# Performance work log

Measured on AMD Instinct MI355X. Metric: run time of the kernel, lower is better.

The kernel has to match this reference:

```python
import jax, jax.numpy as jnp
import numpy as np

Nc, Nq = 100000, 20000
Fc, Fq = 300, 768
HID, H, L = 128, 4, 2
D = HID // H
OUT = 8
E = 400000
NT, ET = 2, 3


def setup_inputs() -> dict:
    key = jax.random.key(0)
    ks = jax.random.split(key, 24)
    def n(i, shape, s=1.0):
        return jax.random.normal(ks[i], shape, dtype=jnp.float32) * s
    return {
        'x_context': n(0, (Nc, Fc)),
        'x_question': n(1, (Nq, Fq)),
        'src_q2c': jax.random.randint(ks[2], (E,), 0, Nq),
        'dst_q2c': jax.random.randint(ks[3], (E,), 0, Nc),
        'src_c2c': jax.random.randint(ks[4], (E,), 0, Nc),
        'dst_c2c': jax.random.randint(ks[5], (E,), 0, Nc),
        'src_c2q': jax.random.randint(ks[6], (E,), 0, Nc),
        'dst_c2q': jax.random.randint(ks[7], (E,), 0, Nq),
        'in_W_context': n(8, (Fc, HID), 0.05),
        'in_b_context': jnp.zeros((HID,), jnp.float32),
        'in_W_question': n(9, (Fq, HID), 0.05),
        'in_b_question': jnp.zeros((HID,), jnp.float32),
        'k_W': n(10, (L, NT, HID, HID), 0.05),
        'k_b': jnp.zeros((L, NT, HID), jnp.float32),
        'q_W': n(11, (L, NT, HID, HID), 0.05),
        'q_b': jnp.zeros((L, NT, HID), jnp.float32),
        'v_W': n(12, (L, NT, HID, HID), 0.05),
        'v_b': jnp.zeros((L, NT, HID), jnp.float32),
        'a_W': n(13, (L, NT, HID, HID), 0.05),
        'a_b': jnp.zeros((L, NT, HID), jnp.float32),
        'skip': jnp.ones((L, NT), jnp.float32),
        'a_rel': n(14, (L, ET, H, D, D), 0.1),
        'm_rel': n(15, (L, ET, H, D, D), 0.1),
        'p_rel': jnp.ones((L, ET, H), jnp.float32),
        'out_W': n(16, (HID, OUT), 0.05),
        'out_b': jnp.zeros((OUT,), jnp.float32),
    }


def segment_softmax(logits, seg, num):
    # logits: [E, H], seg: [E] destination node ids
    m = jax.ops.segment_max(logits, seg, num_segments=num)
    m = jnp.where(jnp.isfinite(m), m, 0.0)
    e = jnp.exp(logits - m[seg])
    s = jax.ops.segment_sum(e, seg, num_segments=num)
    return e / (s[seg] + 1e-16)


def reference(x_context, x_question, src_q2c, dst_q2c, src_c2c, dst_c2c,
              src_c2q, dst_c2q, in_W_context, in_b_context, in_W_question,
              in_b_question, k_W, k_b, q_W, q_b, v_W, v_b, a_W, a_b, skip,
              a_rel, m_rel, p_rel, out_W, out_b):
    # node type 0 = 'context', 1 = 'question'
    x = [jax.nn.relu(x_context @ in_W_context + in_b_context),
         jax.nn.relu(x_question @ in_W_question + in_b_question)]
    Ns = [x[0].shape[0], x[1].shape[0]]
    # (src_nt, dst_nt, src_idx, dst_idx) per edge type
    edge_types = [(1, 0, src_q2c, dst_q2c),
                  (0, 0, src_c2c, dst_c2c),
                  (0, 1, src_c2q, dst_c2q)]
    scale = 1.0 / jnp.sqrt(jnp.float32(D))
    for l in range(L):
        k = [(x[nt] @ k_W[l, nt] + k_b[l, nt]).reshape(-1, H, D) for nt in range(NT)]
        q = [(x[nt] @ q_W[l, nt] + q_b[l, nt]).reshape(-1, H, D) for nt in range(NT)]
        v = [(x[nt] @ v_W[l, nt] + v_b[l, nt]).reshape(-1, H, D) for nt in range(NT)]
        agg = [jnp.zeros((Ns[nt], H, D), x[0].dtype) for nt in range(NT)]
        for et, (snt, dnt, src, dst) in enumerate(edge_types):
            k_rel = jnp.einsum('ehd,hdf->ehf', k[snt][src], a_rel[l, et])
            v_rel = jnp.einsum('ehd,hdf->ehf', v[snt][src], m_rel[l, et])
            logits = jnp.einsum('ehd,ehd->eh', q[dnt][dst], k_rel) * p_rel[l, et] * scale
            alpha = segment_softmax(logits, dst, Ns[dnt])  # [E, H]
            agg[dnt] = agg[dnt].at[dst].add(v_rel * alpha[:, :, None])
        for nt in range(NT):
            o = jax.nn.gelu(agg[nt].reshape(Ns[nt], HID), approximate=False)
            o = o @ a_W[l, nt] + a_b[l, nt]
            g = jax.nn.sigmoid(skip[l, nt])
            x[nt] = g * o + (1.0 - g) * x[nt]
    return x[0] @ out_W + out_b
```

## Files before the change

### kernel.cpp

```cpp
#include <hip/hip_runtime.h>

constexpr int NC = 100000;
constexpr int NQ = 20000;
constexpr int FC = 300;
constexpr int FQ = 768;
constexpr int NEDGE = 400000;
constexpr int NTOT = NC + NC + NQ;
constexpr int NTOT2 = NC + NQ;
constexpr int NB0 = (NC + 127) / 128;
constexpr int NB1 = (NQ + 127) / 128;
constexpr int NBALL = NB0 + NB1;
constexpr float SCALE = 0.17677669529663687f;
constexpr float LOG2E = 1.4426950408889634f;

typedef __attribute__((ext_vector_type(8))) short bf16x8;
typedef __attribute__((ext_vector_type(4))) float f32x4;
typedef unsigned short u16;

__device__ __forceinline__ float gelu_f(float x) {
  return 0.5f * x * (1.0f + erff(x * 0.7071067811865476f));
}
__device__ __forceinline__ u16 bf16_rne(float x) {
  unsigned u = __float_as_uint(x);
  unsigned r = u + 0x7fffu + ((u >> 16) & 1u);
  return (u16)(r >> 16);
}
__device__ __forceinline__ float bf16_to_f(u16 h) {
  return __uint_as_float(((unsigned)h) << 16);
}
__device__ __forceinline__ void split2(float x, u16& hi, u16& lo) {
  hi = bf16_rne(x);
  lo = bf16_rne(x - bf16_to_f(hi));
}
__device__ __forceinline__ void splitT(float x, u16& hi, u16& lo) {
  hi = (u16)(__float_as_uint(x) >> 16);
  lo = bf16_rne(x - bf16_to_f(hi));
}

__global__ void k_count3(const int* __restrict__ d0, const int* __restrict__ d1,
                         const int* __restrict__ d2, int* __restrict__ counts) {
  int i = blockIdx.x * 256 + threadIdx.x;
  if (i >= 3 * NEDGE) return;
  int et = i / NEDGE, e = i - et * NEDGE;
  int d = (et == 0) ? d0[e] : (et == 1) ? d1[e] : d2[e];
  int base = (et == 0) ? 0 : (et == 1) ? NC : 2 * NC;
  atomicAdd(&counts[base + d], 1);
}

__global__ void k_scan_block(const int* __restrict__ in, int* __restrict__ out,
                             int* __restrict__ bsum, int n) {
  __shared__ int s[256];
  int tid = threadIdx.x;
  int i = blockIdx.x * 256 + tid;
  int v = (i < n) ? in[i] : 0;
  s[tid] = v;
  __syncthreads();
  for (int off = 1; off < 256; off <<= 1) {
    int t = (tid >= off) ? s[tid - off] : 0;
    __syncthreads();
    s[tid] += t;
    __syncthreads();
  }
  if (i < n) out[i] = s[tid] - v;
  if (tid == 255) bsum[blockIdx.x] = s[255];
}

__global__ void k_scan_sums(int* __restrict__ bsum, int nb) {
  __shared__ int s[1024];
  int tid = threadIdx.x;
  int v = (tid < nb) ? bsum[tid] : 0;
  s[tid] = v;
  __syncthreads();
  for (int off = 1; off < 1024; off <<= 1) {
    int t = (tid >= off) ? s[tid - off] : 0;
    __syncthreads();
    s[tid] += t;
    __syncthreads();
  }
  if (tid < nb) bsum[tid] = s[tid] - v;
}

__global__ void k_scan_add(int* __restrict__ ptr, const int* __restrict__ bsum,
                           int* __restrict__ cursor, int n, int total) {
  int i = blockIdx.x * 256 + threadIdx.x;
  if (i < n) {
    int v = ptr[i] + bsum[blockIdx.x];
    ptr[i] = v;
    cursor[i] = v;
  }
  if (i == 0) ptr[n] = total;
}

__global__ void k_scatter3(const int* __restrict__ s0, const int* __restrict__ s1,
                           const int* __restrict__ s2, const int* __restrict__ d0,
                           const int* __restrict__ d1, const int* __restrict__ d2,
                           int* __restrict__ cursor, int* __restrict__ srcs_out) {
  int i = blockIdx.x * 256 + threadIdx.x;
  if (i >= 3 * NEDGE) return;
  int et = i / NEDGE, e = i - et * NEDGE;
  int d = (et == 0) ? d0[e] : (et == 1) ? d1[e] : d2[e];
  int sv = (et == 0) ? s0[e] : (et == 1) ? s1[e] : s2[e];
  int base = (et == 0) ? 0 : (et == 1) ? NC : 2 * NC;
  int p = atomicAdd(&cursor[base + d], 1);
  srcs_out[p] = sv;
}

__global__ void prep_all(const float* __restrict__ kW, const float* __restrict__ kB,
                         const float* __restrict__ qW, const float* __restrict__ qB,
                         const float* __restrict__ vW, const float* __restrict__ vB,
                         const float* __restrict__ aW, const float* __restrict__ aB,
                         const float* __restrict__ arel, const float* __restrict__ mrel,
                         const float* __restrict__ prel,
                         u16* __restrict__ Bth, u16* __restrict__ Btl,
                         float* __restrict__ biasOut) {
  int i = blockIdx.x;
  int col = threadIdx.x;
  int y = blockIdx.y;
  int l = y / 10, yy = y % 10;
  size_t lw = (size_t)l * 2 * 16384, lb = (size_t)l * 2 * 128;
  size_t le = (size_t)l * 3 * 4096, lp = (size_t)l * 3 * 4;
  const float *W = nullptr, *bb = nullptr, *rel = nullptr, *pr = nullptr;
  float mscale = 1.0f;
  bool fold = false;
  switch (yy) {
    case 0: W = qW + lw; bb = qB + lb; break;
    case 1: fold = true; W = kW + lw; bb = kB + lb; rel = arel + le + 4096; pr = prel + lp + 4; mscale = SCALE; break;
    case 2: fold = true; W = vW + lw; bb = vB + lb; rel = mrel + le + 4096; break;
    case 3: fold = true; W = kW + lw; bb = kB + lb; rel = arel + le + 8192; pr = prel + lp + 8; mscale = SCALE; break;
    case 4: fold = true; W = vW + lw; bb = vB + lb; rel = mrel + le + 8192; break;
    case 5: W = qW + lw + 16384; bb = qB + lb + 128; break;
    case 6: fold = true; W = kW + lw + 16384; bb = kB + lb + 128; rel = arel + le; pr = prel + lp; mscale = SCALE; break;
    case 7: fold = true; W = vW + lw + 16384; bb = vB + lb + 128; rel = mrel + le; break;
    case 8: W = aW + lw; bb = aB + lb; break;
    default: W = aW + lw + 16384; bb = aB + lb + 128; break;
  }
  int colOff = y * 128;
  if (!fold) {
    float v = W[i * 128 + col];
    u16 hi, lo;
    split2(v, hi, lo);
    Bth[(size_t)(colOff + col) * 128 + i] = hi;
    Btl[(size_t)(colOff + col) * 128 + i] = lo;
    if (i == 0) biasOut[colOff + col] = bb[col];
    return;
  }
  int h = col >> 5, f = col & 31;
  float m = (pr ? pr[h] : 1.0f) * mscale;
  float s = 0.0f;
  #pragma unroll
  for (int d = 0; d < 32; ++d)
    s += W[i * 128 + h * 32 + d] * rel[(h * 32 + d) * 32 + f];
  s *= m;
  u16 hi, lo;
  split2(s, hi, lo);
  Bth[(size_t)(colOff + col) * 128 + i] = hi;
  Btl[(size_t)(colOff + col) * 128 + i] = lo;
  if (i == 0) {
    float sb = 0.0f;
    #pragma unroll
    for (int d = 0; d < 32; ++d)
      sb += bb[h * 32 + d] * rel[(h * 32 + d) * 32 + f];
    biasOut[colOff + col] = sb * m;
  }
}

__global__ void split_in(const float* __restrict__ Wc, const float* __restrict__ bc,
                         const float* __restrict__ Wq, const float* __restrict__ bq,
                         u16* __restrict__ Bth, u16* __restrict__ Btl,
                         float* __restrict__ biasOut) {
  int n = blockIdx.x, y = blockIdx.y;
  const float* W = y ? Wq : Wc;
  const float* b = y ? bq : bc;
  int K = y ? FQ : FC, Kp = y ? 768 : 320;
  size_t boff = y ? (size_t)128 * 320 : 0;
  for (int k = threadIdx.x; k < Kp; k += 256) {
    float v = (k < K) ? W[(size_t)k * 128 + n] : 0.0f;
    u16 hi, lo;
    split2(v, hi, lo);
    Bth[boff + (size_t)n * Kp + k] = hi;
    Btl[boff + (size_t)n * Kp + k] = lo;
  }
  if (threadIdx.x == 0) biasOut[(y ? 128 : 0) + n] = b[n];
}

__global__ __launch_bounds__(256) void big_gemm(
    const float* __restrict__ Ac, const float* __restrict__ Aq,
    const u16* __restrict__ Bth, const u16* __restrict__ Btl,
    const float* __restrict__ biasBuf,
    u16* __restrict__ xh_all, u16* __restrict__ xl_all) {
  __shared__ u16 smem[20480];
  constexpr int AHo = 0, ALo = 5120, BHo = 10240, BLo = 15360;
  const int tid = threadIdx.x, lane = tid & 63, wv = tid >> 6;
  const int l15 = lane & 15, g4 = lane >> 4, koff = g4 * 8;
  const int sr = tid >> 1, sc16 = (tid & 1) * 16;

  const int bid = blockIdx.x;
  const int nt = (bid < NB0) ? 0 : 1;
  const int m0 = nt ? (bid - NB0) * 128 : bid * 128;
  const int M = nt ? NQ : NC;
  const int rowbase = nt ? NC : 0;
  const float* A32;
  int K, Kp, biasOff;
  size_t boff;
  if (nt == 0) { A32 = Ac; K = FC; Kp = 320; boff = 0; biasOff = 0; }
  else { A32 = Aq; K = FQ; Kp = 768; boff = (size_t)128 * 320; biasOff = 128; }
  size_t arow = (size_t)(m0 + sr) * K;
  const bool rowokA = (m0 + sr) < M;

  f32x4 acc[2][8];
  #pragma unroll
  for (int mi = 0; mi < 2; ++mi)
    #pragma unroll
    for (int ni = 0; ni < 8; ++ni) acc[mi][ni] = (f32x4){0.f, 0.f, 0.f, 0.f};

  for (int k0 = 0; k0 < K; k0 += 32) {
    float va[16];
    if (rowokA && (k0 + 32 <= K)) {
      const float* ap = A32 + arow + k0 + sc16;
      #pragma unroll
      for (int j = 0; j < 4; ++j) {
        float4 f = *(const float4*)(ap + 4 * j);
        va[4 * j + 0] = f.x; va[4 * j + 1] = f.y; va[4 * j + 2] = f.z; va[4 * j + 3] = f.w;
      }
    } else {
      #pragma unroll
      for (int j = 0; j < 16; ++j) {
        int kc = k0 + sc16 + j;
        va[j] = (rowokA && kc < K) ? A32[arow + kc] : 0.0f;
      }
    }
    {
      alignas(16) u16 hv[16], lv[16];
      #pragma unroll
      for (int j = 0; j < 16; ++j) splitT(va[j], hv[j], lv[j]);
      *(uint4*)&smem[AHo + sr * 40 + sc16] = *(const uint4*)&hv[0];
      *(uint4*)&smem[AHo + sr * 40 + sc16 + 8] = *(const uint4*)&hv[8];
      *(uint4*)&smem[ALo + sr * 40 + sc16] = *(const uint4*)&lv[0];
      *(uint4*)&smem[ALo + sr * 40 + sc16 + 8] = *(const uint4*)&lv[8];
    }
    {
      const u16* bp = Bth + boff + (size_t)sr * Kp + k0 + sc16;
      *(uint4*)&smem[BHo + sr * 40 + sc16] = *(const uint4*)bp;
      *(uint4*)&smem[BHo + sr * 40 + sc16 + 8] = *(const uint4*)(bp + 8);
      const u16* lp = Btl + boff + (size_t)sr * Kp + k0 + sc16;
      *(uint4*)&smem[BLo + sr * 40 + sc16] = *(const uint4*)lp;
      *(uint4*)&smem[BLo + sr * 40 + sc16 + 8] = *(const uint4*)(lp + 8);
    }
    __syncthreads();

    bf16x8 a_h[2], a_l[2];
    #pragma unroll
    for (int mi = 0; mi < 2; ++mi) {
      int row = wv * 32 + mi * 16 + l15;
      a_h[mi] = *(const bf16x8*)&smem[AHo + row * 40 + koff];
      a_l[mi] = *(const bf16x8*)&smem[ALo + row * 40 + koff];
    }
    #pragma unroll
    for (int ni = 0; ni < 8; ++ni) {
      int col = ni * 16 + l15;
      bf16x8 b_h = *(const bf16x8*)&smem[BHo + col * 40 + koff];
      bf16x8 b_l = *(const bf16x8*)&smem[BLo + col * 40 + koff];
      #pragma unroll
      for (int mi = 0; mi < 2; ++mi) {
        acc[mi][ni] = __builtin_amdgcn_mfma_f32_16x16x32_bf16(a_h[mi], b_h, acc[mi][ni], 0, 0, 0);
        acc[mi][ni] = __builtin_amdgcn_mfma_f32_16x16x32_bf16(a_l[mi], b_h, acc[mi][ni], 0, 0, 0);
        acc[mi][ni] = __builtin_amdgcn_mfma_f32_16x16x32_bf16(a_h[mi], b_l, acc[mi][ni], 0, 0, 0);
      }
    }
    __syncthreads();
  }

  #pragma unroll
  for (int mi = 0; mi < 2; ++mi)
    #pragma unroll
    for (int ni = 0; ni < 8; ++ni) {
      float bi = biasBuf[biasOff + ni * 16 + l15];
      #pragma unroll
      for (int rr = 0; rr < 4; ++rr)
        acc[mi][ni][rr] = fmaxf(acc[mi][ni][rr] + bi, 0.0f);
    }

  const int wrow = tid >> 2, wseg = tid & 3;
  #pragma unroll
  for (int ph = 0; ph < 2; ++ph) {
    #pragma unroll
    for (int h = 0; h < 2; ++h) {
      if (ph || h) __syncthreads();
      if ((wv >> 1) == h) {
        #pragma unroll
        for (int mi = 0; mi < 2; ++mi) {
          int rl = (wv & 1) * 32 + mi * 16 + g4 * 4;
          #pragma unroll
          for (int ni = 0; ni < 8; ++ni) {
            #pragma unroll
            for (int rr = 0; rr < 4; ++rr) {
              u16 hh, ll;
              split2(acc[mi][ni][rr], hh, ll);
              smem[(rl + rr) * 136 + ni * 16 + l15] = ph ? ll : hh;
            }
          }
        }
      }
      __syncthreads();
      int grow = m0 + h * 64 + wrow;
      if (grow < M) {
        u16* dstp = ph ? xl_all : xh_all;
        uint4* dst = (uint4*)&dstp[(size_t)(rowbase + grow) * 128 + wseg * 32];
        const uint4* src = (const uint4*)&smem[wrow * 136 + wseg * 32];
        #pragma unroll
        for (int j = 0; j < 4; ++j) dst[j] = src[j];
      }
    }
  }
}

__global__ __launch_bounds__(256) void aproj_gemm(
    const u16* __restrict__ Ag,
    const u16* __restrict__ Bth, const u16* __restrict__ Btl,
    const float* __restrict__ biasBuf,
    u16* __restrict__ xh_all, u16* __restrict__ xl_all,
    const float* __restrict__ skip, int l) {
  __shared__ u16 smem[15360];
  constexpr int AH = 0, BHo = 5120, BLo = 10240;
  const int tid = threadIdx.x, lane = tid & 63, wv = tid >> 6;
  const int l15 = lane & 15, g4 = lane >> 4, koff = g4 * 8;
  const int sr = tid >> 1, sc = (tid & 1) * 16;

  const int bid = blockIdx.x;
  const int nt = (bid < NB0) ? 0 : 1;
  const int m0 = nt ? (bid - NB0) * 128 : bid * 128;
  const int M = nt ? NQ : NC;
  const int rowbase = nt ? NC : 0;
  const size_t boff = (size_t)(8 + nt) * 16384;
  const int biasOff = (8 + nt) * 128;
  const bool rowok = (m0 + sr) < M;

  f32x4 acc[2][8];
  #pragma unroll
  for (int mi = 0; mi < 2; ++mi)
    #pragma unroll
    for (int ni = 0; ni < 8; ++ni) acc[mi][ni] = (f32x4){0.f, 0.f, 0.f, 0.f};

  for (int k0 = 0; k0 < 128; k0 += 32) {
    uint4 h0 = {0, 0, 0, 0}, h1 = {0, 0, 0, 0};
    if (rowok) {
      const u16* ap = Ag + (size_t)(rowbase + m0 + sr) * 128 + k0 + sc;
      h0 = *(const uint4*)ap;
      h1 = *(const uint4*)(ap + 8);
    }
    *(uint4*)&smem[AH + sr * 40 + sc] = h0;
    *(uint4*)&smem[AH + sr * 40 + sc + 8] = h1;
    {
      const u16* bp = Bth + boff + (size_t)sr * 128 + k0 + sc;
      *(uint4*)&smem[BHo + sr * 40 + sc] = *(const uint4*)bp;
      *(uint4*)&smem[BHo + sr * 40 + sc + 8] = *(const uint4*)(bp + 8);
      const u16* lp = Btl + boff + (size_t)sr * 128 + k0 + sc;
      *(uint4*)&smem[BLo + sr * 40 + sc] = *(const uint4*)lp;
      *(uint4*)&smem[BLo + sr * 40 + sc + 8] = *(const uint4*)(lp + 8);
    }
    __syncthreads();

    bf16x8 a_h[2];
    #pragma unroll
    for (int mi = 0; mi < 2; ++mi) {
      int row = wv * 32 + mi * 16 + l15;
      a_h[mi] = *(const bf16x8*)&smem[AH + row * 40 + koff];
    }
    #pragma unroll
    for (int ni = 0; ni < 8; ++ni) {
      int col = ni * 16 + l15;
      bf16x8 b_h = *(const bf16x8*)&smem[BHo + col * 40 + koff];
      bf16x8 b_l = *(const bf16x8*)&smem[BLo + col * 40 + koff];
      #pragma unroll
      for (int mi = 0; mi < 2; ++mi) {
        acc[mi][ni] = __builtin_amdgcn_mfma_f32_16x16x32_bf16(a_h[mi], b_h, acc[mi][ni], 0, 0, 0);
        acc[mi][ni] = __builtin_amdgcn_mfma_f32_16x16x32_bf16(a_h[mi], b_l, acc[mi][ni], 0, 0, 0);
      }
    }
    __syncthreads();
  }

  float g = 1.0f / (1.0f + __expf(-skip[l * 2 + nt]));

  #pragma unroll
  for (int mi = 0; mi < 2; ++mi) {
    #pragma unroll
    for (int ni = 0; ni < 8; ++ni) {
      int colL = ni * 16 + l15;
      float bi = biasBuf[biasOff + colL];
      #pragma unroll
      for (int rr = 0; rr < 4; ++rr) {
        int row = m0 + wv * 32 + mi * 16 + g4 * 4 + rr;
        float o = acc[mi][ni][rr] + bi;
        if (row < M) {
          size_t idx = (size_t)(rowbase + row) * 128 + colL;
          float xo = bf16_to_f(xh_all[idx]) + bf16_to_f(xl_all[idx]);
          o = g * o + (1.0f - g) * xo;
        }
        acc[mi][ni][rr] = o;
      }
    }
  }

  const int wrow = tid >> 2, wseg = tid & 3;
  #pragma unroll
  for (int ph = 0; ph < 2; ++ph) {
    #pragma unroll
    for (int h = 0; h < 2; ++h) {
      if (ph || h) __syncthreads();
      if ((wv >> 1) == h) {
        #pragma unroll
        for (int mi = 0; mi < 2; ++mi) {
          int rl = (wv & 1) * 32 + mi * 16 + g4 * 4;
          #pragma unroll
          for (int ni = 0; ni < 8; ++ni) {
            #pragma unroll
            for (int rr = 0; rr < 4; ++rr) {
              u16 hh, ll;
              split2(acc[mi][ni][rr], hh, ll);
              smem[(rl + rr) * 136 + ni * 16 + l15] = ph ? ll : hh;
            }
          }
        }
      }
      __syncthreads();
      int grow = m0 + h * 64 + wrow;
      if (grow < M) {
        u16* dstp = ph ? xl_all : xh_all;
        uint4* dst = (uint4*)&dstp[(size_t)(rowbase + grow) * 128 + wseg * 32];
        const uint4* src = (const uint4*)&smem[wrow * 136 + wseg * 32];
        #pragma unroll
        for (int j = 0; j < 4; ++j) dst[j] = src[j];
      }
    }
  }
}

__global__ __launch_bounds__(256) void proj_all(
    const u16* __restrict__ xh_all,
    const u16* __restrict__ Bth, const float* __restrict__ biasBuf,
    u16* __restrict__ q_all, u16* __restrict__ kvA,
    u16* __restrict__ kvB1, u16* __restrict__ kvB2, int last) {
  int bid = blockIdx.x, y = blockIdx.y;
  int nt = (bid < NB0) ? 0 : 1;
  if (nt == 1 && y >= 3) return;
  if (last) {
    if (nt == 0 && y >= 3) return;
    if (nt == 1 && y == 0) return;
  }
  __shared__ u16 smem[10240];
  constexpr int AH = 0, BH = 5120;
  int m0 = nt ? (bid - NB0) * 128 : bid * 128;
  int M = nt ? NQ : NC;
  int abase = nt ? NC : 0;
  int bslab = nt ? 5 + y : y;
  u16* cp; int ld, cb, crowbase;
  if (nt == 0) {
    switch (y) {
      case 0: cp = q_all; ld = 128; cb = 0; crowbase = 0; break;
      case 1: cp = kvB1; ld = 256; cb = 0; crowbase = 0; break;
      case 2: cp = kvB1; ld = 256; cb = 128; crowbase = 0; break;
      case 3: cp = kvB2; ld = 256; cb = 0; crowbase = 0; break;
      default: cp = kvB2; ld = 256; cb = 128; crowbase = 0; break;
    }
  } else {
    switch (y) {
      case 0: cp = q_all; ld = 128; cb = 0; crowbase = NC; break;
      case 1: cp = kvA; ld = 256; cb = 0; crowbase = 0; break;
      default: cp = kvA; ld = 256; cb = 128; crowbase = 0; break;
    }
  }
  const int tid = threadIdx.x, lane = tid & 63, wv = tid >> 6;
  const int l15 = lane & 15, g4 = lane >> 4, koff = g4 * 8;
  const int sr = tid >> 1, sc = (tid & 1) * 16;
  const bool rowok = (m0 + sr) < M;

  f32x4 acc[2][8];
  #pragma unroll
  for (int mi = 0; mi < 2; ++mi)
    #pragma unroll
    for (int ni = 0; ni < 8; ++ni) acc[mi][ni] = (f32x4){0.f, 0.f, 0.f, 0.f};

  for (int k0 = 0; k0 < 128; k0 += 32) {
    uint4 h0 = {0, 0, 0, 0}, h1 = {0, 0, 0, 0};
    if (rowok) {
      const u16* ap = xh_all + (size_t)(abase + m0 + sr) * 128 + k0 + sc;
      h0 = *(const uint4*)ap;
      h1 = *(const uint4*)(ap + 8);
    }
    *(uint4*)&smem[AH + sr * 40 + sc] = h0;
    *(uint4*)&smem[AH + sr * 40 + sc + 8] = h1;
    {
      const u16* bp = Bth + (size_t)(bslab * 128 + sr) * 128 + k0 + sc;
      *(uint4*)&smem[BH + sr * 40 + sc] = *(const uint4*)bp;
      *(uint4*)&smem[BH + sr * 40 + sc + 8] = *(const uint4*)(bp + 8);
    }
    __syncthreads();

    bf16x8 a_h[2];
    #pragma unroll
    for (int mi = 0; mi < 2; ++mi) {
      int row = wv * 32 + mi * 16 + l15;
      a_h[mi] = *(const bf16x8*)&smem[AH + row * 40 + koff];
    }
    #pragma unroll
    for (int ni = 0; ni < 8; ++ni) {
      int col = ni * 16 + l15;
      bf16x8 b_h = *(const bf16x8*)&smem[BH + col * 40 + koff];
      #pragma unroll
      for (int mi = 0; mi < 2; ++mi)
        acc[mi][ni] = __builtin_amdgcn_mfma_f32_16x16x32_bf16(a_h[mi], b_h, acc[mi][ni], 0, 0, 0);
    }
    __syncthreads();
  }

  const int wrow = tid >> 2, wseg = tid & 3;
  #pragma unroll
  for (int h = 0; h < 2; ++h) {
    if (h) __syncthreads();
    if ((wv >> 1) == h) {
      #pragma unroll
      for (int mi = 0; mi < 2; ++mi) {
        int rl = (wv & 1) * 32 + mi * 16 + g4 * 4;
        #pragma unroll
        for (int ni = 0; ni < 8; ++ni) {
          float bi = biasBuf[bslab * 128 + ni * 16 + l15];
          #pragma unroll
          for (int rr = 0; rr < 4; ++rr)
            smem[(rl + rr) * 136 + ni * 16 + l15] = bf16_rne(acc[mi][ni][rr] + bi);
        }
      }
    }
    __syncthreads();
    int grow = m0 + h * 64 + wrow;
    if (grow < M) {
      uint4* dst = (uint4*)&cp[(size_t)(crowbase + grow) * ld + cb + wseg * 32];
      const uint4* src = (const uint4*)&smem[wrow * 136 + wseg * 32];
      #pragma unroll
      for (int j = 0; j < 4; ++j) dst[j] = src[j];
    }
  }
}

__device__ __forceinline__ void attn_seg(
    const u16* __restrict__ kv, int start, int end,
    const int* __restrict__ srcs, const float q8[8], int lane, float accO[8]) {
  if (start >= end) return;
  float sum = 0.0f;
  float acc[8];
  #pragma unroll
  for (int i = 0; i < 8; ++i) acc[i] = 0.0f;
  const int half = lane >> 5;
  const int sub = lane & 31;
  const int bsrc = lane & 44;
  for (int e = start; e < end; e += 4) {
    int e0 = e + half;
    int e1 = e + 2 + half;
    bool v0 = e0 < end, v1 = e1 < end;
    int c0 = v0 ? e0 : end - 1;
    int c1 = v1 ? e1 : end - 1;
    int s0 = srcs[c0];
    int s1 = srcs[c1];
    uint4 u0 = *(const uint4*)&kv[(size_t)s0 * 256 + sub * 8];
    uint4 u1 = *(const uint4*)&kv[(size_t)s1 * 256 + sub * 8];
    float r0[8], r1[8];
    r0[0] = bf16_to_f((u16)(u0.x & 0xffffu)); r0[1] = bf16_to_f((u16)(u0.x >> 16));
    r0[2] = bf16_to_f((u16)(u0.y & 0xffffu)); r0[3] = bf16_to_f((u16)(u0.y >> 16));
    r0[4] = bf16_to_f((u16)(u0.z & 0xffffu)); r0[5] = bf16_to_f((u16)(u0.z >> 16));
    r0[6] = bf16_to_f((u16)(u0.w & 0xffffu)); r0[7] = bf16_to_f((u16)(u0.w >> 16));
    r1[0] = bf16_to_f((u16)(u1.x & 0xffffu)); r1[1] = bf16_to_f((u16)(u1.x >> 16));
    r1[2] = bf16_to_f((u16)(u1.y & 0xffffu)); r1[3] = bf16_to_f((u16)(u1.y >> 16));
    r1[4] = bf16_to_f((u16)(u1.z & 0xffffu)); r1[5] = bf16_to_f((u16)(u1.z >> 16));
    r1[6] = bf16_to_f((u16)(u1.w & 0xffffu)); r1[7] = bf16_to_f((u16)(u1.w >> 16));
    float p0 = q8[0] * r0[0];
    float p1 = q8[0] * r1[0];
    #pragma unroll
    for (int i = 1; i < 8; ++i) {
      p0 = fmaf(q8[i], r0[i], p0);
      p1 = fmaf(q8[i], r1[i], p1);
    }
    p0 += __shfl_xor(p0, 1);
    p1 += __shfl_xor(p1, 1);
    p0 += __shfl_xor(p0, 2);
    p1 += __shfl_xor(p1, 2);
    p0 = fminf(p0, 100.0f);
    p1 = fminf(p1, 100.0f);
    float w0 = v0 ? exp2f(p0) : 0.0f;
    float w1 = v1 ? exp2f(p1) : 0.0f;
    float wB0 = __shfl(w0, bsrc);
    float wB1 = __shfl(w1, bsrc);
    sum += wB0 + wB1;
    #pragma unroll
    for (int i = 0; i < 8; ++i) {
      acc[i] = fmaf(wB0, r0[i], acc[i]);
      acc[i] = fmaf(wB1, r1[i], acc[i]);
    }
  }
  sum += __shfl_xor(sum, 32);
  #pragma unroll
  for (int i = 0; i < 8; ++i) acc[i] += __shfl_xor(acc[i], 32);
  float inv = 1.0f / (sum + 1e-16f);
  #pragma unroll
  for (int i = 0; i < 8; ++i) accO[i] = fmaf(acc[i], inv, accO[i]);
}

__global__ __launch_bounds__(256) void attn_all(
    const u16* __restrict__ q_all, const u16* __restrict__ kvA,
    const u16* __restrict__ kvB1, const u16* __restrict__ kvB2,
    const int* __restrict__ ptr_all, const int* __restrict__ srcs_all,
    u16* __restrict__ agg_g, int ncap) {
  int wave = threadIdx.x >> 6, lane = threadIdx.x & 63;
  int node = blockIdx.x * 4 + wave;
  if (node >= ncap) return;
  int sub = lane & 31;
  float q8[8];
  #pragma unroll
  for (int i = 0; i < 8; ++i) q8[i] = 0.0f;
  if (sub < 16) {
    uint4 u = *(const uint4*)&q_all[(size_t)node * 128 + sub * 8];
    q8[0] = bf16_to_f((u16)(u.x & 0xffffu)) * LOG2E; q8[1] = bf16_to_f((u16)(u.x >> 16)) * LOG2E;
    q8[2] = bf16_to_f((u16)(u.y & 0xffffu)) * LOG2E; q8[3] = bf16_to_f((u16)(u.y >> 16)) * LOG2E;
    q8[4] = bf16_to_f((u16)(u.z & 0xffffu)) * LOG2E; q8[5] = bf16_to_f((u16)(u.z >> 16)) * LOG2E;
    q8[6] = bf16_to_f((u16)(u.w & 0xffffu)) * LOG2E; q8[7] = bf16_to_f((u16)(u.w >> 16)) * LOG2E;
  }
  float accO[8];
  #pragma unroll
  for (int i = 0; i < 8; ++i) accO[i] = 0.0f;
  if (node < NC) {
    attn_seg(kvA, ptr_all[node], ptr_all[node + 1], srcs_all, q8, lane, accO);
    attn_seg(kvB1, ptr_all[NC + node], ptr_all[NC + node + 1], srcs_all, q8, lane, accO);
  } else {
    int idx = 2 * NC + (node - NC);
    attn_seg(kvB2, ptr_all[idx], ptr_all[idx + 1], srcs_all, q8, lane, accO);
  }
  if (lane >= 16 && lane < 32) {
    int j = lane - 16;
    alignas(16) u16 hv[8];
    #pragma unroll
    for (int i = 0; i < 8; ++i) hv[i] = bf16_rne(gelu_f(accO[i]));
    *(uint4*)&agg_g[(size_t)node * 128 + j * 8] = *(const uint4*)hv;
  }
}

__global__ __launch_bounds__(256) void gemm_out(const u16* __restrict__ Xh,
                                                const u16* __restrict__ Xl,
                                                const float* __restrict__ W,
                                                const float* __restrict__ b,
                                                float* __restrict__ out, int M) {
  __shared__ float Ws[1024];
  __shared__ float As[32][129];
  int tid = threadIdx.x;
  int m0 = blockIdx.x * 32;
  *(float4*)&Ws[tid * 4] = *(const float4*)&W[tid * 4];
  {
    int r = tid >> 3;
    int c0 = (tid & 7) * 16;
    if (m0 + r < M) {
      const u16* hp = Xh + (size_t)(m0 + r) * 128 + c0;
      const u16* lp = Xl + (size_t)(m0 + r) * 128 + c0;
      #pragma unroll
      for (int j = 0; j < 16; ++j) As[r][c0 + j] = bf16_to_f(hp[j]) + bf16_to_f(lp[j]);
    } else {
      #pragma unroll
      for (int j = 0; j < 16; ++j) As[r][c0 + j] = 0.0f;
    }
  }
  __syncthreads();
  int r = tid >> 3, c = tid & 7;
  float sum = b[c];
  #pragma unroll 16
  for (int k = 0; k < 128; ++k) sum = fmaf(As[r][k], Ws[k * 8 + c], sum);
  if (m0 + r < M) out[(size_t)(m0 + r) * 8 + c] = sum;
}

static inline size_t align256(size_t x) { return (x + 255) & ~(size_t)255; }

extern "C" void kernel_launch(void* const* d_in, const int* in_sizes, int n_in,
                              void* d_out, int out_size, void* d_ws, size_t ws_size,
                              hipStream_t stream) {
  const float* x_context = (const float*)d_in[0];
  const float* x_question = (const float*)d_in[1];
  const int* src_q2c = (const int*)d_in[2];
  const int* dst_q2c = (const int*)d_in[3];
  const int* src_c2c = (const int*)d_in[4];
  const int* dst_c2c = (const int*)d_in[5];
  const int* src_c2q = (const int*)d_in[6];
  const int* dst_c2q = (const int*)d_in[7];
  const float* inWc = (const float*)d_in[8];
  const float* inbc = (const float*)d_in[9];
  const float* inWq = (const float*)d_in[10];
  const float* inbq = (const float*)d_in[11];
  const float* kW = (const float*)d_in[12];
  const float* kB = (const float*)d_in[13];
  const float* qW = (const float*)d_in[14];
  const float* qB = (const float*)d_in[15];
  const float* vW = (const float*)d_in[16];
  const float* vB = (const float*)d_in[17];
  const float* aW = (const float*)d_in[18];
  const float* aB = (const float*)d_in[19];
  const float* skip = (const float*)d_in[20];
  const float* arel = (const float*)d_in[21];
  const float* mrel = (const float*)d_in[22];
  const float* prel = (const float*)d_in[23];
  const float* outW = (const float*)d_in[24];
  const float* outb = (const float*)d_in[25];

  char* base = (char*)d_ws;
  size_t off = 0;
  auto carve = [&](size_t bytes) -> void* {
    void* p = base + off;
    off = align256(off + bytes);
    return p;
  };
  u16* xh_all = (u16*)carve((size_t)NTOT2 * 128 * 2);
  u16* xl_all = (u16*)carve((size_t)NTOT2 * 128 * 2);
  u16* q_all = (u16*)carve((size_t)NTOT2 * 128 * 2);
  u16* kvA = (u16*)carve((size_t)NQ * 256 * 2);
  u16* kvB1 = (u16*)carve((size_t)NC * 256 * 2);
  u16* kvB2 = (u16*)carve((size_t)NC * 256 * 2);
  u16* agg_g = (u16*)carve((size_t)NTOT2 * 128 * 2);
  u16* Bth = (u16*)carve((size_t)2560 * 128 * 2);
  u16* Btl = (u16*)carve((size_t)2560 * 128 * 2);
  u16* BthI = (u16*)carve((size_t)(320 + 768) * 128 * 2);
  u16* BtlI = (u16*)carve((size_t)(320 + 768) * 128 * 2);
  float* biasBuf = (float*)carve(2560 * 4);
  float* biasIn = (float*)carve(256 * 4);
  int* ptr_all = (int*)carve((size_t)(NTOT + 1) * 4);
  int* srcs_all = (int*)carve((size_t)3 * NEDGE * 4);
  int* counts = (int*)carve((size_t)NTOT * 4);
  int* cursor = (int*)carve((size_t)NTOT * 4);
  int* blksums = (int*)carve(2048 * 4);

  {
    int nb = (NTOT + 255) / 256;
    hipMemsetAsync(counts, 0, (size_t)NTOT * 4, stream);
    k_count3<<<(3 * NEDGE + 255) / 256, 256, 0, stream>>>(dst_q2c, dst_c2c, dst_c2q, counts);
    k_scan_block<<<nb, 256, 0, stream>>>(counts, ptr_all, blksums, NTOT);
    k_scan_sums<<<1, 1024, 0, stream>>>(blksums, nb);
    k_scan_add<<<nb, 256, 0, stream>>>(ptr_all, blksums, cursor, NTOT, 3 * NEDGE);
    k_scatter3<<<(3 * NEDGE + 255) / 256, 256, 0, stream>>>(
        src_q2c, src_c2c, src_c2q, dst_q2c, dst_c2c, dst_c2q, cursor, srcs_all);
  }

  split_in<<<dim3(128, 2), 256, 0, stream>>>(inWc, inbc, inWq, inbq, BthI, BtlI, biasIn);
  prep_all<<<dim3(128, 20), 128, 0, stream>>>(kW, kB, qW, qB, vW, vB, aW, aB,
                                              arel, mrel, prel, Bth, Btl, biasBuf);

  big_gemm<<<NBALL, 256, 0, stream>>>(x_context, x_question, BthI, BtlI, biasIn,
                                      xh_all, xl_all);

  for (int l = 0; l < 2; ++l) {
    const int last = (l == 1);
    const u16* BthL = Bth + (size_t)l * 10 * 128 * 128;
    const u16* BtlL = Btl + (size_t)l * 10 * 128 * 128;
    const float* biasL = biasBuf + (size_t)l * 1280;
    proj_all<<<dim3(NBALL, 5), 256, 0, stream>>>(xh_all, BthL, biasL,
                                                 q_all, kvA, kvB1, kvB2, last);
    int ncap = last ? NC : NTOT2;
    attn_all<<<(ncap + 3) / 4, 256, 0, stream>>>(q_all, kvA, kvB1, kvB2,
                                                 ptr_all, srcs_all, agg_g, ncap);
    aproj_gemm<<<last ? NB0 : NBALL, 256, 0, stream>>>(agg_g, BthL, BtlL, biasL,
                                                       xh_all, xl_all, skip, l);
  }

  gemm_out<<<(NC + 31) / 32, 256, 0, stream>>>(xh_all, xl_all, outW, outb, (float*)d_out, NC);
}
```

Baseline: 728.8 us.

## Load activation tile once and loop over weight slabs in projection kernel

The projection kernel now stages each block's 128x128 activation tile into shared memory once and iterates over all needed weight slabs (q, k, v per edge type) inside the block, instead of launching a separate block per slab that reloads the activation tile. This cuts repeated global reads of activations and the number of blocks, at the cost of larger shared memory use and fewer blocks per launch. The counts memset is also folded into the weight-prep kernel, which is moved ahead of the CSR build to save one launch.

```diff
diff --git a/kernel.cpp b/kernel.cpp
--- a/kernel.cpp
+++ b/kernel.cpp
@@ -112,10 +112,14 @@
                          const float* __restrict__ arel, const float* __restrict__ mrel,
                          const float* __restrict__ prel,
                          u16* __restrict__ Bth, u16* __restrict__ Btl,
-                         float* __restrict__ biasOut) {
+                         float* __restrict__ biasOut, int* __restrict__ counts) {
   int i = blockIdx.x;
   int col = threadIdx.x;
   int y = blockIdx.y;
+  {
+    int gid = (y * 128 + i) * 128 + col;
+    if (gid < NTOT) counts[gid] = 0;
+  }
   int l = y / 10, yy = y % 10;
   size_t lw = (size_t)l * 2 * 16384, lb = (size_t)l * 2 * 128;
   size_t le = (size_t)l * 3 * 4096, lp = (size_t)l * 3 * 4;
@@ -436,108 +440,115 @@
   }
 }
 
-__global__ __launch_bounds__(256) void proj_all(
+__global__ __launch_bounds__(256) void projN(
     const u16* __restrict__ xh_all,
     const u16* __restrict__ Bth, const float* __restrict__ biasBuf,
     u16* __restrict__ q_all, u16* __restrict__ kvA,
     u16* __restrict__ kvB1, u16* __restrict__ kvB2, int last) {
-  int bid = blockIdx.x, y = blockIdx.y;
-  int nt = (bid < NB0) ? 0 : 1;
-  if (nt == 1 && y >= 3) return;
-  if (last) {
-    if (nt == 0 && y >= 3) return;
-    if (nt == 1 && y == 0) return;
-  }
-  __shared__ u16 smem[10240];
-  constexpr int AH = 0, BH = 5120;
-  int m0 = nt ? (bid - NB0) * 128 : bid * 128;
-  int M = nt ? NQ : NC;
-  int abase = nt ? NC : 0;
-  int bslab = nt ? 5 + y : y;
-  u16* cp; int ld, cb, crowbase;
-  if (nt == 0) {
-    switch (y) {
-      case 0: cp = q_all; ld = 128; cb = 0; crowbase = 0; break;
-      case 1: cp = kvB1; ld = 256; cb = 0; crowbase = 0; break;
-      case 2: cp = kvB1; ld = 256; cb = 128; crowbase = 0; break;
-      case 3: cp = kvB2; ld = 256; cb = 0; crowbase = 0; break;
-      default: cp = kvB2; ld = 256; cb = 128; crowbase = 0; break;
-    }
-  } else {
-    switch (y) {
-      case 0: cp = q_all; ld = 128; cb = 0; crowbase = NC; break;
-      case 1: cp = kvA; ld = 256; cb = 0; crowbase = 0; break;
-      default: cp = kvA; ld = 256; cb = 128; crowbase = 0; break;
-    }
-  }
+  __shared__ u16 smem[22528];
+  constexpr int AH = 0, BH = 17408;
   const int tid = threadIdx.x, lane = tid & 63, wv = tid >> 6;
   const int l15 = lane & 15, g4 = lane >> 4, koff = g4 * 8;
-  const int sr = tid >> 1, sc = (tid & 1) * 16;
-  const bool rowok = (m0 + sr) < M;
-
-  f32x4 acc[2][8];
-  #pragma unroll
-  for (int mi = 0; mi < 2; ++mi)
-    #pragma unroll
-    for (int ni = 0; ni < 8; ++ni) acc[mi][ni] = (f32x4){0.f, 0.f, 0.f, 0.f};
-
-  for (int k0 = 0; k0 < 128; k0 += 32) {
-    uint4 h0 = {0, 0, 0, 0}, h1 = {0, 0, 0, 0};
-    if (rowok) {
-      const u16* ap = xh_all + (size_t)(abase + m0 + sr) * 128 + k0 + sc;
-      h0 = *(const uint4*)ap;
-      h1 = *(const uint4*)(ap + 8);
-    }
-    *(uint4*)&smem[AH + sr * 40 + sc] = h0;
-    *(uint4*)&smem[AH + sr * 40 + sc + 8] = h1;
-    {
-      const u16* bp = Bth + (size_t)(bslab * 128 + sr) * 128 + k0 + sc;
-      *(uint4*)&smem[BH + sr * 40 + sc] = *(const uint4*)bp;
-      *(uint4*)&smem[BH + sr * 40 + sc + 8] = *(const uint4*)(bp + 8);
-    }
-    __syncthreads();
-
-    bf16x8 a_h[2];
-    #pragma unroll
-    for (int mi = 0; mi < 2; ++mi) {
-      int row = wv * 32 + mi * 16 + l15;
-      a_h[mi] = *(const bf16x8*)&smem[AH + row * 40 + koff];
-    }
-    #pragma unroll
-    for (int ni = 0; ni < 8; ++ni) {
-      int col = ni * 16 + l15;
-      bf16x8 b_h = *(const bf16x8*)&smem[BH + col * 40 + koff];
-      #pragma unroll
-      for (int mi = 0; mi < 2; ++mi)
-        acc[mi][ni] = __builtin_amdgcn_mfma_f32_16x16x32_bf16(a_h[mi], b_h, acc[mi][ni], 0, 0, 0);
-    }
-    __syncthreads();
-  }
-
-  const int wrow = tid >> 2, wseg = tid & 3;
-  #pragma unroll
-  for (int h = 0; h < 2; ++h) {
-    if (h) __syncthreads();
-    if ((wv >> 1) == h) {
+  const int bid = blockIdx.x;
+  const int nt = (bid < NB0) ? 0 : 1;
+  const int m0 = nt ? (bid - NB0) * 128 : bid * 128;
+  const int M = nt ? NQ : NC;
+  const int abase = nt ? NC : 0;
+  const int nslab = nt ? (last ? 2 : 3) : (last ? 3 : 5);
+
+  {
+    const int sr = tid >> 1, sc = (tid & 1) * 64;
+    if ((m0 + sr) < M) {
+      const u16* ap = xh_all + (size_t)(abase + m0 + sr) * 128 + sc;
+      #pragma unroll
+      for (int j = 0; j < 8; ++j)
+        *(uint4*)&smem[AH + sr * 136 + sc + j * 8] = *(const uint4*)(ap + j * 8);
+    } else {
+      uint4 z = {0, 0, 0, 0};
+      #pragma unroll
+      for (int j = 0; j < 8; ++j)
+        *(uint4*)&smem[AH + sr * 136 + sc + j * 8] = z;
+    }
+  }
+
+  const int srB = tid >> 1, scB = (tid & 1) * 16;
+  for (int s = 0; s < nslab; ++s) {
+    int y = (nt == 1 && last) ? (s + 1) : s;
+    int bslab = nt ? 5 + y : y;
+    u16* cp; int ld, cb, crowbase;
+    if (nt == 0) {
+      switch (y) {
+        case 0: cp = q_all; ld = 128; cb = 0; crowbase = 0; break;
+        case 1: cp = kvB1; ld = 256; cb = 0; crowbase = 0; break;
+        case 2: cp = kvB1; ld = 256; cb = 128; crowbase = 0; break;
+        case 3: cp = kvB2; ld = 256; cb = 0; crowbase = 0; break;
+        default: cp = kvB2; ld = 256; cb = 128; crowbase = 0; break;
+      }
+    } else {
+      switch (y) {
+        case 0: cp = q_all; ld = 128; cb = 0; crowbase = NC; break;
+        case 1: cp = kvA; ld = 256; cb = 0; crowbase = 0; break;
+        default: cp = kvA; ld = 256; cb = 128; crowbase = 0; break;
+      }
+    }
+
+    f32x4 acc[2][8];
+    #pragma unroll
+    for (int mi = 0; mi < 2; ++mi)
+      #pragma unroll
+      for (int ni = 0; ni < 8; ++ni) acc[mi][ni] = (f32x4){0.f, 0.f, 0.f, 0.f};
+
+    #pragma unroll
+    for (int ks = 0; ks < 4; ++ks) {
+      const u16* bp = Bth + (size_t)(bslab * 128 + srB) * 128 + ks * 32 + scB;
+      uint4 b0 = *(const uint4*)bp;
+      uint4 b1 = *(const uint4*)(bp + 8);
+      __syncthreads();
+      *(uint4*)&smem[BH + srB * 40 + scB] = b0;
+      *(uint4*)&smem[BH + srB * 40 + scB + 8] = b1;
+      __syncthreads();
+
+      bf16x8 a_h[2];
       #pragma unroll
       for (int mi = 0; mi < 2; ++mi) {
-        int rl = (wv & 1) * 32 + mi * 16 + g4 * 4;
+        int row = wv * 32 + mi * 16 + l15;
+        a_h[mi] = *(const bf16x8*)&smem[AH + row * 136 + ks * 32 + koff];
+      }
+      #pragma unroll
+      for (int ni = 0; ni < 8; ++ni) {
+        int col = ni * 16 + l15;
+        bf16x8 b_h = *(const bf16x8*)&smem[BH + col * 40 + koff];
         #pragma unroll
-        for (int ni = 0; ni < 8; ++ni) {
-          float bi = biasBuf[bslab * 128 + ni * 16 + l15];
+        for (int mi = 0; mi < 2; ++mi)
+          acc[mi][ni] = __builtin_amdgcn_mfma_f32_16x16x32_bf16(a_h[mi], b_h, acc[mi][ni], 0, 0, 0);
+      }
+    }
+
+    #pragma unroll
+    for (int h = 0; h < 4; ++h) {
+      __syncthreads();
+      if (wv == h) {
+        #pragma unroll
+        for (int mi = 0; mi < 2; ++mi) {
+          int rl = mi * 16 + g4 * 4;
           #pragma unroll
-          for (int rr = 0; rr < 4; ++rr)
-            smem[(rl + rr) * 136 + ni * 16 + l15] = bf16_rne(acc[mi][ni][rr] + bi);
+          for (int ni = 0; ni < 8; ++ni) {
+            float bi = biasBuf[bslab * 128 + ni * 16 + l15];
+            #pragma unroll
+            for (int rr = 0; rr < 4; ++rr)
+              smem[BH + (rl + rr) * 136 + ni * 16 + l15] = bf16_rne(acc[mi][ni][rr] + bi);
+          }
         }
       }
-    }
-    __syncthreads();
-    int grow = m0 + h * 64 + wrow;
-    if (grow < M) {
-      uint4* dst = (uint4*)&cp[(size_t)(crowbase + grow) * ld + cb + wseg * 32];
-      const uint4* src = (const uint4*)&smem[wrow * 136 + wseg * 32];
-      #pragma unroll
-      for (int j = 0; j < 4; ++j) dst[j] = src[j];
+      __syncthreads();
+      int r = tid >> 3, cseg = (tid & 7) * 16;
+      int grow = m0 + h * 32 + r;
+      if (grow < M) {
+        uint4* dst = (uint4*)&cp[(size_t)(crowbase + grow) * ld + cb + cseg];
+        const uint4* src = (const uint4*)&smem[BH + r * 136 + cseg];
+        dst[0] = src[0];
+        dst[1] = src[1];
+      }
     }
   }
 }
@@ -731,9 +742,12 @@
   int* cursor = (int*)carve((size_t)NTOT * 4);
   int* blksums = (int*)carve(2048 * 4);
 
+  split_in<<<dim3(128, 2), 256, 0, stream>>>(inWc, inbc, inWq, inbq, BthI, BtlI, biasIn);
+  prep_all<<<dim3(128, 20), 128, 0, stream>>>(kW, kB, qW, qB, vW, vB, aW, aB,
+                                              arel, mrel, prel, Bth, Btl, biasBuf, counts);
+
   {
     int nb = (NTOT + 255) / 256;
-    hipMemsetAsync(counts, 0, (size_t)NTOT * 4, stream);
     k_count3<<<(3 * NEDGE + 255) / 256, 256, 0, stream>>>(dst_q2c, dst_c2c, dst_c2q, counts);
     k_scan_block<<<nb, 256, 0, stream>>>(counts, ptr_all, blksums, NTOT);
     k_scan_sums<<<1, 1024, 0, stream>>>(blksums, nb);
@@ -742,10 +756,6 @@
         src_q2c, src_c2c, src_c2q, dst_q2c, dst_c2c, dst_c2q, cursor, srcs_all);
   }
 
-  split_in<<<dim3(128, 2), 256, 0, stream>>>(inWc, inbc, inWq, inbq, BthI, BtlI, biasIn);
-  prep_all<<<dim3(128, 20), 128, 0, stream>>>(kW, kB, qW, qB, vW, vB, aW, aB,
-                                              arel, mrel, prel, Bth, Btl, biasBuf);
-
   big_gemm<<<NBALL, 256, 0, stream>>>(x_context, x_question, BthI, BtlI, biasIn,
                                       xh_all, xl_all);
 
@@ -754,8 +764,7 @@
     const u16* BthL = Bth + (size_t)l * 10 * 128 * 128;
     const u16* BtlL = Btl + (size_t)l * 10 * 128 * 128;
     const float* biasL = biasBuf + (size_t)l * 1280;
-    proj_all<<<dim3(NBALL, 5), 256, 0, stream>>>(xh_all, BthL, biasL,
-                                                 q_all, kvA, kvB1, kvB2, last);
+    projN<<<NBALL, 256, 0, stream>>>(xh_all, BthL, biasL, q_all, kvA, kvB1, kvB2, last);
     int ncap = last ? NC : NTOT2;
     attn_all<<<(ncap + 3) / 4, 256, 0, stream>>>(q_all, kvA, kvB1, kvB2,
                                                  ptr_all, srcs_all, agg_g, ncap);
```

New measurement: 715.0 us. Within noise of the previous version (-1.9%).
